# Performance work log

Hardware: AMD Instinct MI355X
Metric: run time of the kernel (lower is better)

Reference implementation:

```python
import jax, jax.numpy as jnp
import numpy as np

N_NODES = 100_000
N_EDGES = 1_600_000
F_IN = 32
F_OUT = 32
DIM = 2
K = 5                      # kernel_size per dim (open spline)
KTOT = K ** DIM            # 25 kernel weight matrices
S = 2 ** DIM               # 4 nonzero linear-B-spline basis terms per edge
NEG_SLOPE = 0.2

# offsets over the 2^DIM corners of the spline cell, [S, DIM]
_OFFSETS = np.array([[(s >> d) & 1 for d in range(DIM)] for s in range(S)], dtype=np.int32)
_STRIDES = np.array([K ** d for d in range(DIM)], dtype=np.int32)


def _spline_basis(pseudo):
    """Degree-1 open B-spline basis. pseudo: [E, DIM] in [0,1].
    Returns basis [E, S] and kernel-weight indices widx [E, S]."""
    offsets = jnp.asarray(_OFFSETS)
    strides = jnp.asarray(_STRIDES)
    p = pseudo * (K - 1)                         # open spline scaling
    fl = jnp.floor(p)
    frac = p - fl                                # [E, DIM]
    b = jnp.where(offsets[None] == 0, 1.0 - frac[:, None, :], frac[:, None, :])
    basis = jnp.prod(b, axis=-1)                 # [E, S]
    idx = jnp.clip(fl.astype(jnp.int32)[:, None, :] + offsets[None], 0, K - 1)
    widx = jnp.sum(idx * strides, axis=-1)       # [E, S] in [0, KTOT)
    return basis, widx


def setup_inputs() -> dict:
    key = jax.random.key(0)
    ks = jax.random.split(key, 7)
    x = jax.random.normal(ks[0], (N_NODES, F_IN), dtype=jnp.float32)
    edge_index = jax.random.randint(ks[1], (2, N_EDGES), 0, N_NODES)
    pseudo = jax.random.uniform(ks[2], (N_EDGES, DIM), dtype=jnp.float32)
    bound = 1.0 / np.sqrt(KTOT * F_IN)           # matches reset_parameters uniform(size, ...)
    weight = jax.random.uniform(ks[3], (KTOT, F_IN, F_OUT), jnp.float32, -bound, bound)
    root_weight = jax.random.uniform(ks[4], (F_IN, F_OUT), jnp.float32, -bound, bound)
    att_weight = jax.random.uniform(ks[5], (2 * F_OUT,), jnp.float32, -bound, bound)
    bias = jax.random.uniform(ks[6], (F_OUT,), jnp.float32, -bound, bound)
    return {"x": x, "edge_index": edge_index, "pseudo": pseudo, "weight": weight,
            "root_weight": root_weight, "att_weight": att_weight, "bias": bias}


def reference(x, edge_index, pseudo, weight, root_weight, att_weight, bias):
    row, col = edge_index[0], edge_index[1]      # row = target, col = source
    basis, widx = _spline_basis(pseudo)          # [E,S], [E,S]

    # Precompute x @ W_k for every kernel weight: [N, KTOT, F_OUT]
    xw = jnp.einsum('nf,kfo->nko', x, weight)
    flat = col[:, None] * KTOT + widx            # [E, S] flat (node, kernel) index
    gathered = xw.reshape(-1, F_OUT)[flat]       # [E, S, F_OUT]
    msg = jnp.einsum('es,esf->ef', basis, gathered)  # spline-weighted edge messages

    x_root = x @ root_weight                     # [N, F_OUT]

    # GAT-style attention logits: cat([x_root[row], msg]) . att_weight
    alpha = x_root[row] @ att_weight[:F_OUT] + msg @ att_weight[F_OUT:]
    alpha = jnp.where(alpha > 0, alpha, NEG_SLOPE * alpha)  # leaky relu

    # segment softmax over incoming edges of each target node
    amax = jax.ops.segment_max(alpha, row, num_segments=N_NODES)
    amax = jnp.where(jnp.isfinite(amax), amax, 0.0)
    ex = jnp.exp(alpha - amax[row])
    denom = jax.ops.segment_sum(ex, row, num_segments=N_NODES)
    att = ex / (denom[row] + 1e-16)

    out = jax.ops.segment_sum(msg * att[:, None], row, num_segments=N_NODES)
    return out + x_root + bias
```

## Files before the change

### kernel.cpp

```cpp
#include <hip/hip_runtime.h>
#include <stdint.h>

#define N_NODES 100000
#define N_EDGES 1600000
#define NBLK_SCAN 391

typedef __attribute__((ext_vector_type(8))) short short8;
typedef __attribute__((ext_vector_type(4))) float float4v;

__device__ __forceinline__ unsigned short f32_to_bf16(float f) {
  uint32_t u = __float_as_uint(f);
  u += 0x7fffu + ((u >> 16) & 1u);
  return (unsigned short)(u >> 16);
}
__device__ __forceinline__ float bf16_to_f32(unsigned short h) {
  return __uint_as_float(((uint32_t)h) << 16);
}

__global__ __launch_bounds__(256) void k_zero(
    const float* __restrict__ weight, const float* __restrict__ root_w,
    int* __restrict__ deg, unsigned short* __restrict__ wbf,
    unsigned short* __restrict__ xw, float* __restrict__ ydot) {
  int tid = threadIdx.x;
  int b = blockIdx.x;
  int i = b * 256 + tid;
  if (i < N_NODES) deg[i] = 0;
  if (b < 100) {
    int e = i;
    int km = e >> 10;
    int rem = e & 1023;
    int kk = rem >> 5;
    int fo = rem & 31;
    int t = km * 2 + (fo >> 4);
    int c = fo & 15;
    int q = kk >> 3, j = kk & 7;
    wbf[((t * 4 + q) * 16 + c) * 8 + j] = f32_to_bf16(weight[e]);
  } else if (b == 100) {
    for (int idx = tid; idx < 1024; idx += 256) {
      int kk = idx >> 5;
      int fo = idx & 31;
      int t = 50 + (fo >> 4);
      int q = kk >> 3, j = kk & 7;
      wbf[((t * 4 + q) * 16 + (fo & 15)) * 8 + j] = f32_to_bf16(root_w[idx]);
    }
  } else if (b == 101) {
    if (tid < 400) ((unsigned int*)(xw + 80000000))[tid] = 0u;
    if (tid < 16) ydot[2500000 + tid] = 0.f;
  }
}

__global__ __launch_bounds__(256) void k1_xw(
    const float* __restrict__ x, const unsigned short* __restrict__ wbf,
    const int* __restrict__ ei, const float* __restrict__ att_w,
    const float* __restrict__ bias,
    int* __restrict__ deg, unsigned short* __restrict__ rank,
    unsigned short* __restrict__ xw, float* __restrict__ out,
    uint2* __restrict__ od, float* __restrict__ ydot) {
  __shared__ __align__(16) unsigned short ot[16 * 808];
  __shared__ float xr[16][33];
  __shared__ float att2s[32];
  int tid = threadIdx.x;
  int b = blockIdx.x;

  if (tid < 32) att2s[tid] = att_w[32 + tid];

  int e = b * 256 + tid;
  int rk = atomicAdd(&deg[ei[e]], 1);

  int wave = tid >> 6, lane = tid & 63;
  int quad = lane >> 4, c16 = lane & 15;
  int n0 = b * 16;
  const float* xp = x + (size_t)(n0 + c16) * 32 + quad * 8;
  float4 a0 = *reinterpret_cast<const float4*>(xp);
  float4 a1 = *reinterpret_cast<const float4*>(xp + 4);
  short8 af;
  af[0] = (short)f32_to_bf16(a0.x); af[1] = (short)f32_to_bf16(a0.y);
  af[2] = (short)f32_to_bf16(a0.z); af[3] = (short)f32_to_bf16(a0.w);
  af[4] = (short)f32_to_bf16(a1.x); af[5] = (short)f32_to_bf16(a1.y);
  af[6] = (short)f32_to_bf16(a1.z); af[7] = (short)f32_to_bf16(a1.w);

  for (int t = wave; t < 52; t += 4) {
    short8 bf = *reinterpret_cast<const short8*>(wbf + ((t * 4 + quad) * 16 + c16) * 8);
    float4v acc = {0.f, 0.f, 0.f, 0.f};
    acc = __builtin_amdgcn_mfma_f32_16x16x32_bf16(af, bf, acc, 0, 0, 0);
    if (t < 50) {
      int cg = t * 16 + c16;
#pragma unroll
      for (int r = 0; r < 4; r++) ot[(quad * 4 + r) * 808 + cg] = f32_to_bf16(acc[r]);
    } else {
      int f = (t - 50) * 16 + c16;
#pragma unroll
      for (int r = 0; r < 4; r++) xr[quad * 4 + r][f] = acc[r];
    }
  }
  __syncthreads();

  const uint4* src = (const uint4*)ot;
  uint4* dst = (uint4*)(xw + (size_t)n0 * 800);
  for (int i = tid; i < 1600; i += 256) {
    int r = i / 100;
    int c = i - r * 100;
    dst[r * 100 + c] = src[r * 101 + c];
  }
  for (int idx = tid; idx < 512; idx += 256) {
    int n = idx >> 5, f = idx & 31;
    out[(n0 + n) * 32 + f] = xr[n][f] + bias[f];
  }
  for (int idx = tid; idx < 400; idx += 256) {
    int nd = idx / 25;
    int km = idx - nd * 25;
    const unsigned short* orow = ot + nd * 808 + km * 32;
    float s = 0.f;
#pragma unroll
    for (int ff = 0; ff < 32; ff++) s += bf16_to_f32(orow[ff]) * att2s[ff];
    ydot[(size_t)(n0 + nd) * 25 + km] = s;
  }
  if (tid < 16) {
    float s = 0.f;
#pragma unroll
    for (int f = 0; f < 32; f++) s += xr[tid][f] * att_w[f];
    od[n0 + tid].y = __float_as_uint(s);
  }
  rank[e] = (unsigned short)rk;
}

__global__ __launch_bounds__(256) void kscan1(const int* __restrict__ deg,
                                              int* __restrict__ incl,
                                              int* __restrict__ bsum) {
  __shared__ int s[256];
  int tid = threadIdx.x;
  int i = blockIdx.x * 256 + tid;
  int v = (i < N_NODES) ? deg[i] : 0;
  s[tid] = v;
  __syncthreads();
  for (int d = 1; d < 256; d <<= 1) {
    int t = (tid >= d) ? s[tid - d] : 0;
    __syncthreads();
    s[tid] += t;
    __syncthreads();
  }
  if (i < N_NODES) incl[i] = s[tid];
  if (tid == 255) bsum[blockIdx.x] = s[255];
}

__global__ __launch_bounds__(512) void kscan2(const int* __restrict__ bsum,
                                              int* __restrict__ bbase) {
  __shared__ int s[512];
  int tid = threadIdx.x;
  int v = (tid < NBLK_SCAN) ? bsum[tid] : 0;
  s[tid] = v;
  __syncthreads();
  for (int d = 1; d < 512; d <<= 1) {
    int t = (tid >= d) ? s[tid - d] : 0;
    __syncthreads();
    s[tid] += t;
    __syncthreads();
  }
  if (tid < NBLK_SCAN) bbase[tid] = s[tid] - v;
}

__global__ __launch_bounds__(256) void kscan3(const int* __restrict__ deg,
                                              int* __restrict__ offs,
                                              const int* __restrict__ bbase,
                                              uint2* __restrict__ od) {
  int i = blockIdx.x * 256 + threadIdx.x;
  if (i < N_NODES) {
    int v = offs[i] - deg[i] + bbase[i >> 8];
    offs[i] = v;
    od[i].x = (unsigned int)v;
  }
  if (i == 0) offs[N_NODES] = N_EDGES;
}

__global__ __launch_bounds__(256) void kscatter(
    const int* __restrict__ ei, const float* __restrict__ pseudo,
    const uint2* __restrict__ od, const unsigned short* __restrict__ rank,
    const float* __restrict__ ydot,
    unsigned int* __restrict__ eidx, uint2* __restrict__ ecoef) {
  int e = blockIdx.x * 256 + threadIdx.x;
  int r = ei[e];
  int c = ei[N_EDGES + e];
  float p0 = pseudo[2 * e] * 4.f;
  float p1 = pseudo[2 * e + 1] * 4.f;
  int rk = rank[e];
  uint2 v = od[r];
  float fl0 = floorf(p0), fl1 = floorf(p1);
  float fr0 = p0 - fl0, fr1 = p1 - fl1;
  int i0 = (int)fl0, i1 = (int)fl1;
  int w0 = min(i0, 4) + 5 * min(i1, 4);
  int w2 = min(i0, 4) + 5 * min(i1 + 1, 4);
  const float* yb = ydot + (size_t)c * 25;
  float y0 = yb[w0], y1 = yb[w0 + 1];
  float y2 = yb[w2], y3 = yb[w2 + 1];
  float c0 = 1.f - fr0, c1 = 1.f - fr1;
  float b0 = c0 * c1, b1 = fr0 * c1, b2 = c0 * fr1, b3 = fr0 * fr1;
  float alpha = __uint_as_float(v.y) + b0 * y0 + b1 * y1 + b2 * y2 + b3 * y3;
  alpha = alpha > 0.f ? alpha : 0.2f * alpha;
  float ex = __expf(alpha);
  int pos = (int)v.x + rk;
  uint2 pk;
  pk.x = (unsigned int)f32_to_bf16(b0 * ex) |
         ((unsigned int)f32_to_bf16(b1 * ex) << 16);
  pk.y = (unsigned int)f32_to_bf16(b2 * ex) |
         ((unsigned int)f32_to_bf16(b3 * ex) << 16);
  ecoef[pos] = pk;
  eidx[pos] = (unsigned int)c | ((unsigned int)w0 << 17) |
              ((unsigned int)w2 << 22);
}

__global__ __launch_bounds__(256) void k2_csr(
    const int* __restrict__ offs, const unsigned int* __restrict__ eidx,
    const uint2* __restrict__ ecoef, const unsigned short* __restrict__ xw,
    float* __restrict__ out) {
  int tid = threadIdx.x;
  int wave = tid >> 6, lane = tid & 63;
  int node = blockIdx.x * 4 + wave;
  if (node >= N_NODES) return;
  int f = lane & 31, half = lane >> 5;
  int s0 = offs[node], s1 = offs[node + 1];
  const unsigned short* xwf = xw + f;
  float accA = 0.f, accB = 0.f, denA = 0.f, denB = 0.f;
  int i = s0 + half;

  for (; i + 6 < s1; i += 8) {
    unsigned int id[4];
    uint2 cf[4];
    id[0] = eidx[i];     id[1] = eidx[i + 2];
    id[2] = eidx[i + 4]; id[3] = eidx[i + 6];
    cf[0] = ecoef[i];     cf[1] = ecoef[i + 2];
    cf[2] = ecoef[i + 4]; cf[3] = ecoef[i + 6];
    float g0[4], g1[4], g2[4], g3[4];
#pragma unroll
    for (int u = 0; u < 4; u++) {
      const unsigned short* base = xwf + (size_t)(id[u] & 0x1FFFF) * 800;
      int o0 = ((id[u] >> 17) & 31) * 32;
      int o2 = ((id[u] >> 22) & 31) * 32;
      g0[u] = bf16_to_f32(base[o0]);
      g1[u] = bf16_to_f32(base[o0 + 32]);
      g2[u] = bf16_to_f32(base[o2]);
      g3[u] = bf16_to_f32(base[o2 + 32]);
    }
#pragma unroll
    for (int u = 0; u < 4; u++) {
      float q0 = __uint_as_float(cf[u].x << 16);
      float q1 = __uint_as_float(cf[u].x & 0xffff0000u);
      float q2 = __uint_as_float(cf[u].y << 16);
      float q3 = __uint_as_float(cf[u].y & 0xffff0000u);
      float m = q0 * g0[u] + q1 * g1[u] + q2 * g2[u] + q3 * g3[u];
      float d = (q0 + q1) + (q2 + q3);
      if (u & 1) { accB += m; denB += d; } else { accA += m; denA += d; }
    }
  }
  for (; i < s1; i += 2) {
    unsigned int idv = eidx[i];
    uint2 cfv = ecoef[i];
    const unsigned short* base = xwf + (size_t)(idv & 0x1FFFF) * 800;
    int o0 = ((idv >> 17) & 31) * 32;
    int o2 = ((idv >> 22) & 31) * 32;
    float g0 = bf16_to_f32(base[o0]);
    float g1 = bf16_to_f32(base[o0 + 32]);
    float g2 = bf16_to_f32(base[o2]);
    float g3 = bf16_to_f32(base[o2 + 32]);
    float q0 = __uint_as_float(cfv.x << 16);
    float q1 = __uint_as_float(cfv.x & 0xffff0000u);
    float q2 = __uint_as_float(cfv.y << 16);
    float q3 = __uint_as_float(cfv.y & 0xffff0000u);
    accA += q0 * g0 + q1 * g1 + q2 * g2 + q3 * g3;
    denA += (q0 + q1) + (q2 + q3);
  }

  float acc = accA + accB;
  float den = denA + denB;
  acc += __shfl_xor(acc, 32);
  den += __shfl_xor(den, 32);
  if (half == 0) out[node * 32 + f] += acc / (den + 1e-16f);
}

extern "C" void kernel_launch(void* const* d_in, const int* in_sizes, int n_in,
                              void* d_out, int out_size, void* d_ws, size_t ws_size,
                              hipStream_t stream) {
  const float* x      = (const float*)d_in[0];
  const int*   ei     = (const int*)d_in[1];
  const float* pseudo = (const float*)d_in[2];
  const float* weight = (const float*)d_in[3];
  const float* root_w = (const float*)d_in[4];
  const float* att_w  = (const float*)d_in[5];
  const float* bias   = (const float*)d_in[6];
  float* out = (float*)d_out;

  char* ws = (char*)d_ws;
  unsigned short* xw   = (unsigned short*)ws;
  float* ydot          = (float*)(ws + 160001600);
  uint2* od            = (uint2*)(ws + 170001664);
  unsigned short* wbf  = (unsigned short*)(ws + 170801664);
  int* deg             = (int*)(ws + 170854912);
  int* offs            = (int*)(ws + 171254912);
  int* bsum            = (int*)(ws + 171654928);
  int* bbase           = (int*)(ws + 171656528);
  unsigned short* rank = (unsigned short*)(ws + 171658128);
  uint2* ecoef         = (uint2*)(ws + 174858128);
  unsigned int* eidx   = (unsigned int*)(ws + 187658128);

  hipLaunchKernelGGL(k_zero, dim3(NBLK_SCAN), dim3(256), 0, stream,
                     weight, root_w, deg, wbf, xw, ydot);
  hipLaunchKernelGGL(k1_xw, dim3(6250), dim3(256), 0, stream,
                     x, wbf, ei, att_w, bias, deg, rank, xw, out, od, ydot);
  hipLaunchKernelGGL(kscan1, dim3(NBLK_SCAN), dim3(256), 0, stream, deg, offs, bsum);
  hipLaunchKernelGGL(kscan2, dim3(1), dim3(512), 0, stream, bsum, bbase);
  hipLaunchKernelGGL(kscan3, dim3(NBLK_SCAN), dim3(256), 0, stream, deg, offs, bbase, od);
  hipLaunchKernelGGL(kscatter, dim3(6250), dim3(256), 0, stream,
                     ei, pseudo, od, rank, ydot, eidx, ecoef);
  hipLaunchKernelGGL(k2_csr, dim3(25000), dim3(256), 0, stream,
                     offs, eidx, ecoef, xw, out);
}
```

Measured before the change: 378.1 us.

## Fold attention vector into weights, drop LDS staging, pack per-cell logit table

The attention projection W_k·att is precomputed into extra MFMA tiles, so the per-node logit dots come straight from the MFMA instead of a second pass over bf16 xw in shared memory. The MFMA operands are swapped so each lane writes its xw, out and logit results directly to global memory, which removes the LDS staging buffer and the block barrier. A new kernel packs the four corner logits of each spline cell into one bf16 uint2, so kscatter does a single 8-byte gather instead of four scattered float loads. The costs are an extra launch, reduced logit precision, and direct global stores that are less coalesced than before. ydot now aliases the ecoef buffer.

Result: slower. 411.6 us (+8.9%).

```diff
diff --git a/kernel.cpp b/kernel.cpp
--- a/kernel.cpp
+++ b/kernel.cpp
@@ -19,33 +19,40 @@
 
 __global__ __launch_bounds__(256) void k_zero(
     const float* __restrict__ weight, const float* __restrict__ root_w,
+    const float* __restrict__ att_w,
     int* __restrict__ deg, unsigned short* __restrict__ wbf,
-    unsigned short* __restrict__ xw, float* __restrict__ ydot) {
+    unsigned short* __restrict__ xw) {
   int tid = threadIdx.x;
   int b = blockIdx.x;
   int i = b * 256 + tid;
   if (i < N_NODES) deg[i] = 0;
   if (b < 100) {
     int e = i;
-    int km = e >> 10;
-    int rem = e & 1023;
-    int kk = rem >> 5;
-    int fo = rem & 31;
-    int t = km * 2 + (fo >> 4);
-    int c = fo & 15;
-    int q = kk >> 3, j = kk & 7;
-    wbf[((t * 4 + q) * 16 + c) * 8 + j] = f32_to_bf16(weight[e]);
+    int t = e >> 9, rem = e & 511;
+    int q = rem >> 7, row = (rem >> 3) & 15, j = rem & 7;
+    int km = t >> 1, fin = q * 8 + j, fo = (t & 1) * 16 + row;
+    wbf[e] = f32_to_bf16(weight[(km * 32 + fin) * 32 + fo]);
   } else if (b == 100) {
     for (int idx = tid; idx < 1024; idx += 256) {
-      int kk = idx >> 5;
-      int fo = idx & 31;
-      int t = 50 + (fo >> 4);
-      int q = kk >> 3, j = kk & 7;
-      wbf[((t * 4 + q) * 16 + (fo & 15)) * 8 + j] = f32_to_bf16(root_w[idx]);
+      int t = 50 + (idx >> 9), rem = idx & 511;
+      int q = rem >> 7, row = (rem >> 3) & 15, j = rem & 7;
+      int fin = q * 8 + j, fo = (t - 50) * 16 + row;
+      wbf[t * 512 + rem] = f32_to_bf16(root_w[fin * 32 + fo]);
+    }
+    for (int idx = tid; idx < 1024; idx += 256) {
+      int t = 52 + (idx >> 9), rem = idx & 511;
+      int q = rem >> 7, row = (rem >> 3) & 15, j = rem & 7;
+      int fin = q * 8 + j, km = (t - 52) * 16 + row;
+      float s = 0.f;
+      if (km < 25) {
+#pragma unroll
+        for (int fo = 0; fo < 32; fo++)
+          s += weight[(km * 32 + fin) * 32 + fo] * att_w[32 + fo];
+      }
+      wbf[t * 512 + rem] = f32_to_bf16(s);
     }
   } else if (b == 101) {
     if (tid < 400) ((unsigned int*)(xw + 80000000))[tid] = 0u;
-    if (tid < 16) ydot[2500000 + tid] = 0.f;
   }
 }
 
@@ -56,13 +63,8 @@
     int* __restrict__ deg, unsigned short* __restrict__ rank,
     unsigned short* __restrict__ xw, float* __restrict__ out,
     uint2* __restrict__ od, float* __restrict__ ydot) {
-  __shared__ __align__(16) unsigned short ot[16 * 808];
-  __shared__ float xr[16][33];
-  __shared__ float att2s[32];
   int tid = threadIdx.x;
   int b = blockIdx.x;
-
-  if (tid < 32) att2s[tid] = att_w[32 + tid];
 
   int e = b * 256 + tid;
   int rk = atomicAdd(&deg[ei[e]], 1);
@@ -70,7 +72,8 @@
   int wave = tid >> 6, lane = tid & 63;
   int quad = lane >> 4, c16 = lane & 15;
   int n0 = b * 16;
-  const float* xp = x + (size_t)(n0 + c16) * 32 + quad * 8;
+  int node = n0 + c16;
+  const float* xp = x + (size_t)node * 32 + quad * 8;
   float4 a0 = *reinterpret_cast<const float4*>(xp);
   float4 a1 = *reinterpret_cast<const float4*>(xp + 4);
   short8 af;
@@ -79,47 +82,42 @@
   af[4] = (short)f32_to_bf16(a1.x); af[5] = (short)f32_to_bf16(a1.y);
   af[6] = (short)f32_to_bf16(a1.z); af[7] = (short)f32_to_bf16(a1.w);
 
-  for (int t = wave; t < 52; t += 4) {
+  float rsum = 0.f;
+  int nt = (wave < 2) ? 14 : 13;
+  for (int idx = 0; idx < nt; idx++) {
+    int t = (idx < 13) ? (wave * 13 + idx) : (52 + wave);
     short8 bf = *reinterpret_cast<const short8*>(wbf + ((t * 4 + quad) * 16 + c16) * 8);
     float4v acc = {0.f, 0.f, 0.f, 0.f};
-    acc = __builtin_amdgcn_mfma_f32_16x16x32_bf16(af, bf, acc, 0, 0, 0);
+    acc = __builtin_amdgcn_mfma_f32_16x16x32_bf16(bf, af, acc, 0, 0, 0);
     if (t < 50) {
-      int cg = t * 16 + c16;
+      uint2 pk;
+      pk.x = (unsigned int)f32_to_bf16(acc[0]) |
+             ((unsigned int)f32_to_bf16(acc[1]) << 16);
+      pk.y = (unsigned int)f32_to_bf16(acc[2]) |
+             ((unsigned int)f32_to_bf16(acc[3]) << 16);
+      *reinterpret_cast<uint2*>(xw + (size_t)node * 800 + t * 16 + quad * 4) = pk;
+    } else if (t < 52) {
+      int gfo = (t - 50) * 16 + quad * 4;
+      float4 bi = *reinterpret_cast<const float4*>(bias + gfo);
+      float4 o;
+      o.x = acc[0] + bi.x; o.y = acc[1] + bi.y;
+      o.z = acc[2] + bi.z; o.w = acc[3] + bi.w;
+      *reinterpret_cast<float4*>(out + (size_t)node * 32 + gfo) = o;
+      float4 aw = *reinterpret_cast<const float4*>(att_w + gfo);
+      rsum += acc[0] * aw.x + acc[1] * aw.y + acc[2] * aw.z + acc[3] * aw.w;
+    } else {
+      int kmb = (t - 52) * 16 + quad * 4;
 #pragma unroll
-      for (int r = 0; r < 4; r++) ot[(quad * 4 + r) * 808 + cg] = f32_to_bf16(acc[r]);
-    } else {
-      int f = (t - 50) * 16 + c16;
-#pragma unroll
-      for (int r = 0; r < 4; r++) xr[quad * 4 + r][f] = acc[r];
-    }
-  }
-  __syncthreads();
-
-  const uint4* src = (const uint4*)ot;
-  uint4* dst = (uint4*)(xw + (size_t)n0 * 800);
-  for (int i = tid; i < 1600; i += 256) {
-    int r = i / 100;
-    int c = i - r * 100;
-    dst[r * 100 + c] = src[r * 101 + c];
-  }
-  for (int idx = tid; idx < 512; idx += 256) {
-    int n = idx >> 5, f = idx & 31;
-    out[(n0 + n) * 32 + f] = xr[n][f] + bias[f];
-  }
-  for (int idx = tid; idx < 400; idx += 256) {
-    int nd = idx / 25;
-    int km = idx - nd * 25;
-    const unsigned short* orow = ot + nd * 808 + km * 32;
-    float s = 0.f;
-#pragma unroll
-    for (int ff = 0; ff < 32; ff++) s += bf16_to_f32(orow[ff]) * att2s[ff];
-    ydot[(size_t)(n0 + nd) * 25 + km] = s;
-  }
-  if (tid < 16) {
-    float s = 0.f;
-#pragma unroll
-    for (int f = 0; f < 32; f++) s += xr[tid][f] * att_w[f];
-    od[n0 + tid].y = __float_as_uint(s);
+      for (int r2 = 0; r2 < 4; r2++) {
+        int km = kmb + r2;
+        if (km < 25) ydot[(size_t)node * 25 + km] = acc[r2];
+      }
+    }
+  }
+  if (wave == 3) {
+    rsum += __shfl_xor(rsum, 16);
+    rsum += __shfl_xor(rsum, 32);
+    if (lane < 16) od[node].y = __float_as_uint(rsum);
   }
   rank[e] = (unsigned short)rk;
 }
@@ -172,10 +170,23 @@
   if (i == 0) offs[N_NODES] = N_EDGES;
 }
 
+__global__ __launch_bounds__(256) void k_ydq(const float* __restrict__ ydot,
+                                             uint2* __restrict__ ydq) {
+  int idx = blockIdx.x * 256 + threadIdx.x;
+  int n = idx >> 4, cell = idx & 15;
+  int i1 = cell >> 2, i0 = cell & 3;
+  const float* bb = ydot + (size_t)n * 25 + i1 * 5 + i0;
+  float y0 = bb[0], y1 = bb[1], y2 = bb[5], y3 = bb[6];
+  uint2 pk;
+  pk.x = (unsigned int)f32_to_bf16(y0) | ((unsigned int)f32_to_bf16(y1) << 16);
+  pk.y = (unsigned int)f32_to_bf16(y2) | ((unsigned int)f32_to_bf16(y3) << 16);
+  ydq[idx] = pk;
+}
+
 __global__ __launch_bounds__(256) void kscatter(
     const int* __restrict__ ei, const float* __restrict__ pseudo,
     const uint2* __restrict__ od, const unsigned short* __restrict__ rank,
-    const float* __restrict__ ydot,
+    const uint2* __restrict__ ydq,
     unsigned int* __restrict__ eidx, uint2* __restrict__ ecoef) {
   int e = blockIdx.x * 256 + threadIdx.x;
   int r = ei[e];
@@ -187,17 +198,19 @@
   float fl0 = floorf(p0), fl1 = floorf(p1);
   float fr0 = p0 - fl0, fr1 = p1 - fl1;
   int i0 = (int)fl0, i1 = (int)fl1;
-  int w0 = min(i0, 4) + 5 * min(i1, 4);
-  int w2 = min(i0, 4) + 5 * min(i1 + 1, 4);
-  const float* yb = ydot + (size_t)c * 25;
-  float y0 = yb[w0], y1 = yb[w0 + 1];
-  float y2 = yb[w2], y3 = yb[w2 + 1];
+  uint2 yq = ydq[c * 16 + i1 * 4 + i0];
+  float y0 = __uint_as_float(yq.x << 16);
+  float y1 = __uint_as_float(yq.x & 0xffff0000u);
+  float y2 = __uint_as_float(yq.y << 16);
+  float y3 = __uint_as_float(yq.y & 0xffff0000u);
   float c0 = 1.f - fr0, c1 = 1.f - fr1;
   float b0 = c0 * c1, b1 = fr0 * c1, b2 = c0 * fr1, b3 = fr0 * fr1;
   float alpha = __uint_as_float(v.y) + b0 * y0 + b1 * y1 + b2 * y2 + b3 * y3;
   alpha = alpha > 0.f ? alpha : 0.2f * alpha;
   float ex = __expf(alpha);
   int pos = (int)v.x + rk;
+  int w0 = i0 + 5 * i1;
+  int w2 = w0 + 5;
   uint2 pk;
   pk.x = (unsigned int)f32_to_bf16(b0 * ex) |
          ((unsigned int)f32_to_bf16(b1 * ex) << 16);
@@ -290,26 +303,28 @@
 
   char* ws = (char*)d_ws;
   unsigned short* xw   = (unsigned short*)ws;
-  float* ydot          = (float*)(ws + 160001600);
-  uint2* od            = (uint2*)(ws + 170001664);
-  unsigned short* wbf  = (unsigned short*)(ws + 170801664);
-  int* deg             = (int*)(ws + 170854912);
-  int* offs            = (int*)(ws + 171254912);
-  int* bsum            = (int*)(ws + 171654928);
-  int* bbase           = (int*)(ws + 171656528);
-  unsigned short* rank = (unsigned short*)(ws + 171658128);
-  uint2* ecoef         = (uint2*)(ws + 174858128);
-  unsigned int* eidx   = (unsigned int*)(ws + 187658128);
+  uint2* ydq           = (uint2*)(ws + 160001600);
+  uint2* od            = (uint2*)(ws + 172801600);
+  unsigned short* wbf  = (unsigned short*)(ws + 173601600);
+  int* deg             = (int*)(ws + 173656896);
+  int* offs            = (int*)(ws + 174056896);
+  int* bsum            = (int*)(ws + 174456912);
+  int* bbase           = (int*)(ws + 174458512);
+  unsigned short* rank = (unsigned short*)(ws + 174460112);
+  uint2* ecoef         = (uint2*)(ws + 177660112);
+  float* ydot          = (float*)(ws + 177660112);
+  unsigned int* eidx   = (unsigned int*)(ws + 190460112);
 
   hipLaunchKernelGGL(k_zero, dim3(NBLK_SCAN), dim3(256), 0, stream,
-                     weight, root_w, deg, wbf, xw, ydot);
+                     weight, root_w, att_w, deg, wbf, xw);
   hipLaunchKernelGGL(k1_xw, dim3(6250), dim3(256), 0, stream,
                      x, wbf, ei, att_w, bias, deg, rank, xw, out, od, ydot);
   hipLaunchKernelGGL(kscan1, dim3(NBLK_SCAN), dim3(256), 0, stream, deg, offs, bsum);
   hipLaunchKernelGGL(kscan2, dim3(1), dim3(512), 0, stream, bsum, bbase);
   hipLaunchKernelGGL(kscan3, dim3(NBLK_SCAN), dim3(256), 0, stream, deg, offs, bbase, od);
+  hipLaunchKernelGGL(k_ydq, dim3(6250), dim3(256), 0, stream, ydot, ydq);
   hipLaunchKernelGGL(kscatter, dim3(6250), dim3(256), 0, stream,
-                     ei, pseudo, od, rank, ydot, eidx, ecoef);
+                     ei, pseudo, od, rank, ydq, eidx, ecoef);
   hipLaunchKernelGGL(k2_csr, dim3(25000), dim3(256), 0, stream,
                      offs, eidx, ecoef, xw, out);
 }
```
